# Kernel tuning notes

Hardware: AMD Instinct MI355X
Metric: run time of the kernel (lower is better)

## Reference

```python
import jax, jax.numpy as jnp
import numpy as np

NUM_HEADS = 8
DIM_IN = 512
DIM_OUT = 512


def setup_inputs() -> dict:
    key = jax.random.key(0)
    k1, k2, k3, k4, k5, k6 = jax.random.split(key, 6)
    B, T, J, C = 8, 243, 17, DIM_IN
    H = NUM_HEADS
    x = jax.random.normal(k1, (B, T, J, C), dtype=jnp.float32)
    # external attention map over temporal axis per joint: [B,H,J,T,T]
    att_map = jax.random.uniform(k2, (B, H, J, T, T), dtype=jnp.float32)
    weight = jax.random.uniform(k3, (1,), dtype=jnp.float32)
    # learned params (torch Linear stored here as [in,out] so y = x @ W)
    W_qkv = jax.random.normal(k4, (C, 3 * C), dtype=jnp.float32) * (C ** -0.5)
    W_proj = jax.random.normal(k5, (C, DIM_OUT), dtype=jnp.float32) * (C ** -0.5)
    b_proj = jax.random.normal(k6, (DIM_OUT,), dtype=jnp.float32) * 0.02
    return {"x": x, "att_map": att_map, "weight": weight,
            "W_qkv": W_qkv, "W_proj": W_proj, "b_proj": b_proj}


def reference(x, att_map, weight, W_qkv, W_proj, b_proj):
    B, T, J, C = x.shape
    H = NUM_HEADS
    hd = C // H
    scale = hd ** -0.5
    qkv = (x @ W_qkv).reshape(B, T, J, 3, H, hd)
    # permute(3,0,4,1,2,5) then transpose(2,3) -> [3,B,H,J,T,hd]
    qkv = jnp.transpose(qkv, (3, 0, 4, 2, 1, 5))
    q, k, v = qkv[0], qkv[1], qkv[2]
    attn = jax.nn.softmax(jnp.einsum('bhjtd,bhjsd->bhjts', q, k) * scale, axis=-1)
    attn = weight * attn + (1.0 - weight) * att_map  # dropout is identity (p=0 / eval)
    out = jnp.einsum('bhjts,bhjsd->bhjtd', attn, v)  # [B,H,J,T,hd]
    out = jnp.transpose(out, (0, 3, 2, 1, 4)).reshape(B, T, J, H * hd)
    return out @ W_proj + b_proj
```

## Files before the change

kernel.cpp:

```cpp
#include <hip/hip_runtime.h>
#include <hip/hip_bf16.h>
#include <cstddef>
#include <cstdint>

#define NHEADS 8
#define TT 243
#define JJ 17
#define BB 8
#define CC 512
#define HD 64
#define MROWS 33048
#define TJ 4131
#define HJ 136

typedef __attribute__((ext_vector_type(8))) short bf16x8;
typedef __attribute__((ext_vector_type(4))) float f32x4;
typedef __attribute__((ext_vector_type(4), aligned(4))) float f32x4u;

__device__ __forceinline__ unsigned short f2bf(float f) {
    return __builtin_bit_cast(unsigned short, __float2bfloat16(f));
}
__device__ __forceinline__ float b2f(unsigned short u) {
    return __uint_as_float(((unsigned)u) << 16);
}
__device__ __forceinline__ void async16(const void* g, void* l) {
    __builtin_amdgcn_global_load_lds(
        (const __attribute__((address_space(1))) void*)g,
        (__attribute__((address_space(3))) void*)l, 16, 0, 0);
}

__global__ __launch_bounds__(256) void convert_x(
    const float* __restrict__ in, unsigned short* __restrict__ out, int n4)
{
    for (int i = blockIdx.x * 256 + threadIdx.x; i < n4; i += gridDim.x * 256) {
        const float4 v = *(const float4*)(in + (size_t)i * 4);
        ushort4 o;
        o.x = f2bf(v.x); o.y = f2bf(v.y); o.z = f2bf(v.z); o.w = f2bf(v.w);
        *(ushort4*)(out + (size_t)i * 4) = o;
    }
}

__global__ __launch_bounds__(256) void transpose_w(
    const float* __restrict__ src, unsigned short* __restrict__ dst, int N)
{
    __shared__ unsigned short tile[64][65];
    const int tid = threadIdx.x;
    const int c = tid & 63, r4 = tid >> 6;
    const int n0 = blockIdx.x << 6, k0 = blockIdx.y << 6;
    #pragma unroll
    for (int p = 0; p < 16; ++p) {
        const int r = (p << 2) + r4;
        tile[r][c] = f2bf(src[(size_t)(k0 + r) * N + n0 + c]);
    }
    __syncthreads();
    #pragma unroll
    for (int p = 0; p < 16; ++p) {
        const int rr = (p << 2) + r4;
        dst[(size_t)(n0 + rr) * 512 + k0 + c] = tile[c][rr];
    }
}

__global__ __launch_bounds__(256) void gemm_qkv(
    const unsigned short* __restrict__ xb, const unsigned short* __restrict__ wt,
    unsigned short* __restrict__ qb, unsigned short* __restrict__ kb,
    unsigned short* __restrict__ vb)
{
    __shared__ __align__(16) char smem[32768];
    char* const A0 = smem;
    char* const A1 = smem + 8192;
    char* const B0 = smem + 16384;
    char* const B1 = smem + 24576;

    const int tid = threadIdx.x;
    const int wave = tid >> 6, lane = tid & 63;
    const int m0 = blockIdx.y << 7, n0 = blockIdx.x << 7;
    const int wr = wave >> 1, wc = wave & 1;

    f32x4 acc[4][4];
    #pragma unroll
    for (int i = 0; i < 4; ++i)
        #pragma unroll
        for (int j = 0; j < 4; ++j) acc[i][j] = (f32x4){0.f, 0.f, 0.f, 0.f};

    const int srow = lane >> 2;
    const int sbyte = (lane & 3) << 4;
    const int arow0 = (wave << 5) + srow;
    const int arow1 = arow0 + 16;
    const size_t am0 = (size_t)min(m0 + arow0, MROWS - 1);
    const size_t am1 = (size_t)min(m0 + arow1, MROWS - 1);
    const char* xbb = (const char*)xb;
    const char* wtb = (const char*)wt;

#define STAGEQ(Ad, Bd, k0) do { \
    async16(xbb + (am0 * 512 + (k0)) * 2 + sbyte, (Ad) + ((wave << 5) << 6)); \
    async16(xbb + (am1 * 512 + (k0)) * 2 + sbyte, (Ad) + (((wave << 5) + 16) << 6)); \
    async16(wtb + ((size_t)(n0 + arow0) * 512 + (k0)) * 2 + sbyte, (Bd) + ((wave << 5) << 6)); \
    async16(wtb + ((size_t)(n0 + arow1) * 512 + (k0)) * 2 + sbyte, (Bd) + (((wave << 5) + 16) << 6)); \
} while (0)

#define COMPUTEQ(Ap, Bp) do { \
    bf16x8 af[4], bfr[4]; \
    _Pragma("unroll") \
    for (int i = 0; i < 4; ++i) \
        af[i] = *(const bf16x8*)((const unsigned short*)(Ap) + \
            ((wr << 6) + (i << 4) + (lane & 15)) * 32 + ((lane >> 4) << 3)); \
    _Pragma("unroll") \
    for (int j = 0; j < 4; ++j) \
        bfr[j] = *(const bf16x8*)((const unsigned short*)(Bp) + \
            ((wc << 6) + (j << 4) + (lane & 15)) * 32 + ((lane >> 4) << 3)); \
    _Pragma("unroll") \
    for (int i = 0; i < 4; ++i) \
        _Pragma("unroll") \
        for (int j = 0; j < 4; ++j) \
            acc[i][j] = __builtin_amdgcn_mfma_f32_16x16x32_bf16(af[i], bfr[j], acc[i][j], 0, 0, 0); \
} while (0)

    STAGEQ(A0, B0, 0);
    __syncthreads();
    #pragma unroll
    for (int t = 0; t < 16; t += 2) {
        STAGEQ(A1, B1, (t + 1) << 5);
        COMPUTEQ(A0, B0);
        __syncthreads();
        if (t + 2 < 16) STAGEQ(A0, B0, (t + 2) << 5);
        COMPUTEQ(A1, B1);
        __syncthreads();
    }
#undef STAGEQ
#undef COMPUTEQ

    unsigned short (*Cq)[16][72] = (unsigned short (*)[16][72])smem;

    const int nw = n0 + (wc << 6);
    const int which = nw >> 9;
    const int h = (nw >> 6) & 7;
    unsigned short* const dst = which == 0 ? qb : (which == 1 ? kb : vb);
    #pragma unroll
    for (int i = 0; i < 4; ++i) {
        #pragma unroll
        for (int j = 0; j < 4; ++j)
            #pragma unroll
            for (int r = 0; r < 4; ++r)
                Cq[wave][((lane >> 4) << 2) + r][(j << 4) + (lane & 15)] = f2bf(acc[i][j][r]);
        #pragma unroll
        for (int qq = 0; qq < 4; ++qq) {
            const int rr = (qq << 2) + (lane >> 4);
            const int ch = lane & 15;
            const ushort4 val = *(const ushort4*)&Cq[wave][rr][ch << 2];
            const int m = m0 + (wr << 6) + (i << 4) + rr;
            if (m < MROWS) {
                const int b = m / TJ; const int rm = m - b * TJ;
                const int t = rm / JJ; const int jj = rm - t * JJ;
                const size_t base = (((size_t)((b * NHEADS + h) * JJ + jj) * TT + t) << 6) + (ch << 2);
                *(ushort4*)(dst + base) = val;
            }
        }
    }
}

__global__ __launch_bounds__(256) void vtrans(
    const unsigned short* __restrict__ vb, unsigned short* __restrict__ vt)
{
    __shared__ unsigned short TL[64 * 264];
    const int tid = threadIdx.x;
    const int bhj = blockIdx.x;
    const unsigned short* src = vb + (size_t)bhj * TT * HD;

    {
        const int d = tid >> 2, qq = tid & 3;
        *(ushort4*)(TL + d * 264 + 240 + (qq << 2)) = make_ushort4(0, 0, 0, 0);
    }
    __syncthreads();
    #pragma unroll
    for (int p = 0; p < 16; ++p) {
        const int idxq = tid + (p << 8);
        const int t = idxq >> 4;
        if (t < TT) {
            const int d0 = (idxq & 15) << 2;
            const ushort4 u = *(const ushort4*)(src + t * HD + d0);
            TL[(d0 + 0) * 264 + t] = u.x;
            TL[(d0 + 1) * 264 + t] = u.y;
            TL[(d0 + 2) * 264 + t] = u.z;
            TL[(d0 + 3) * 264 + t] = u.w;
        }
    }
    __syncthreads();
    unsigned short* dst = vt + ((size_t)bhj << 14);
    #pragma unroll
    for (int p = 0; p < 8; ++p) {
        const int cw = tid + (p << 8);
        const int d = cw >> 5, c = cw & 31;
        const ushort4 a = *(const ushort4*)(TL + d * 264 + (c << 3));
        const ushort4 bq = *(const ushort4*)(TL + d * 264 + (c << 3) + 4);
        *(ushort4*)(dst + (d << 8) + (c << 3)) = a;
        *(ushort4*)(dst + (d << 8) + (c << 3) + 4) = bq;
    }
}

__global__ __launch_bounds__(256, 2) void attn_mfma(
    const unsigned short* __restrict__ qb, const unsigned short* __restrict__ kb,
    const unsigned short* __restrict__ vt, const float* __restrict__ att,
    const float* __restrict__ wptr, unsigned short* __restrict__ ob)
{
    __shared__ unsigned short ST[64 * 264];

    const int tid = threadIdx.x;
    const int wave = tid >> 6, lane = tid & 63;
    const int tile = blockIdx.x & 3, bhj = blockIdx.x >> 2;
    const int row0 = tile << 6;

    const unsigned short* q = qb + (size_t)bhj * TT * HD;
    const unsigned short* k = kb + (size_t)bhj * TT * HD;
    const float* am = att + (size_t)bhj * TT * TT;
    const float w = wptr[0];

    const int lm = lane & 15, lk = lane >> 4;

    bf16x8 qf[4][2];
    #pragma unroll
    for (int mi = 0; mi < 4; ++mi) {
        const int r = min(row0 + (mi << 4) + lm, TT - 1);
        #pragma unroll
        for (int kb2 = 0; kb2 < 2; ++kb2)
            qf[mi][kb2] = *(const bf16x8*)(q + r * HD + (kb2 << 5) + (lk << 3));
    }
    bf16x8 kf[2][4];
    #pragma unroll
    for (int kb2 = 0; kb2 < 2; ++kb2)
        #pragma unroll
        for (int nj = 0; nj < 4; ++nj) {
            const int s = min((wave << 6) + (nj << 4) + lm, TT - 1);
            kf[kb2][nj] = *(const bf16x8*)(k + s * HD + (kb2 << 5) + (lk << 3));
        }

    const int row2 = tid >> 2, part = tid & 3;
    const int trow2 = row0 + row2;
    const float* amr = am + (size_t)min(trow2, TT - 1) * TT;
    float areg[15][4];
    #pragma unroll
    for (int i = 0; i < 15; ++i) {
        const f32x4u av = *(const f32x4u*)(amr + (part << 2) + (i << 4));
        areg[i][0] = av.x; areg[i][1] = av.y; areg[i][2] = av.z; areg[i][3] = av.w;
    }
    float at0 = 0.f, at1 = 0.f, at2 = 0.f;
    if (part == 0) { at0 = amr[240]; at1 = amr[241]; at2 = amr[242]; }

    f32x4 acc[4][4];
    #pragma unroll
    for (int mi = 0; mi < 4; ++mi)
        #pragma unroll
        for (int nj = 0; nj < 4; ++nj) acc[mi][nj] = (f32x4){0.f, 0.f, 0.f, 0.f};
    #pragma unroll
    for (int kb2 = 0; kb2 < 2; ++kb2)
        #pragma unroll
        for (int mi = 0; mi < 4; ++mi)
            #pragma unroll
            for (int nj = 0; nj < 4; ++nj)
                acc[mi][nj] = __builtin_amdgcn_mfma_f32_16x16x32_bf16(qf[mi][kb2], kf[kb2][nj], acc[mi][nj], 0, 0, 0);
    #pragma unroll
    for (int mi = 0; mi < 4; ++mi)
        #pragma unroll
        for (int nj = 0; nj < 4; ++nj)
            #pragma unroll
            for (int r = 0; r < 4; ++r) {
                const int m = (mi << 4) + (lk << 2) + r;
                const int s = (wave << 6) + (nj << 4) + lm;
                ST[m * 264 + s] = f2bf(acc[mi][nj][r] * 0.125f);
            }
    __syncthreads();

    {
        unsigned short* strow = ST + row2 * 264;
        if (trow2 < TT) {
            float mx = -1e30f;
            #pragma unroll
            for (int i = 0; i < 15; ++i) {
                const ushort4 u = *(const ushort4*)(strow + (part << 2) + (i << 4));
                mx = fmaxf(fmaxf(fmaxf(fmaxf(mx, b2f(u.x)), b2f(u.y)), b2f(u.z)), b2f(u.w));
            }
            if (part == 0)
                for (int s = 240; s < TT; ++s) mx = fmaxf(mx, b2f(strow[s]));
            mx = fmaxf(mx, __shfl_xor(mx, 1));
            mx = fmaxf(mx, __shfl_xor(mx, 2));

            float er[15][4];
            float l = 0.f;
            #pragma unroll
            for (int i = 0; i < 15; ++i) {
                const int s0 = (part << 2) + (i << 4);
                const ushort4 u = *(const ushort4*)(strow + s0);
                er[i][0] = __expf(b2f(u.x) - mx);
                er[i][1] = __expf(b2f(u.y) - mx);
                er[i][2] = __expf(b2f(u.z) - mx);
                er[i][3] = __expf(b2f(u.w) - mx);
                l += (er[i][0] + er[i][1]) + (er[i][2] + er[i][3]);
            }
            float et0 = 0.f, et1 = 0.f, et2 = 0.f;
            if (part == 0) {
                et0 = __expf(b2f(strow[240]) - mx);
                et1 = __expf(b2f(strow[241]) - mx);
                et2 = __expf(b2f(strow[242]) - mx);
                l += et0 + et1 + et2;
            }
            l += __shfl_xor(l, 1);
            l += __shfl_xor(l, 2);
            const float sw = w / l, aw = 1.f - w;
            #pragma unroll
            for (int i = 0; i < 15; ++i) {
                const int s0 = (part << 2) + (i << 4);
                ushort4 o;
                o.x = f2bf(er[i][0] * sw + aw * areg[i][0]);
                o.y = f2bf(er[i][1] * sw + aw * areg[i][1]);
                o.z = f2bf(er[i][2] * sw + aw * areg[i][2]);
                o.w = f2bf(er[i][3] * sw + aw * areg[i][3]);
                *(ushort4*)(strow + s0) = o;
            }
            if (part == 0) {
                strow[240] = f2bf(et0 * sw + aw * at0);
                strow[241] = f2bf(et1 * sw + aw * at1);
                strow[242] = f2bf(et2 * sw + aw * at2);
                for (int s = TT; s < 256; ++s) strow[s] = 0;
            }
        } else {
            #pragma unroll
            for (int i = 0; i < 16; ++i)
                *(ushort4*)(strow + (part << 2) + (i << 4)) = make_ushort4(0, 0, 0, 0);
        }
    }
    __syncthreads();

    f32x4 oacc[4];
    #pragma unroll
    for (int nj = 0; nj < 4; ++nj) oacc[nj] = (f32x4){0.f, 0.f, 0.f, 0.f};
    const unsigned short* strow3 = ST + ((wave << 4) + lm) * 264;
    const unsigned short* vtg = vt + ((size_t)bhj << 14);
    #pragma unroll 2
    for (int kb8 = 0; kb8 < 8; ++kb8) {
        const bf16x8 pf = *(const bf16x8*)(strow3 + (kb8 << 5) + (lk << 3));
        #pragma unroll
        for (int nj = 0; nj < 4; ++nj) {
            const int d = (nj << 4) + lm;
            const int chunk = (kb8 << 2) + lk;
            const bf16x8 vf = *(const bf16x8*)(vtg + (d << 8) + (chunk << 3));
            oacc[nj] = __builtin_amdgcn_mfma_f32_16x16x32_bf16(pf, vf, oacc[nj], 0, 0, 0);
        }
    }

    const int b = bhj / HJ;
    const int hj = bhj - b * HJ;
    const int h = hj / JJ;
    const int j = hj - h * JJ;
    #pragma unroll
    for (int r = 0; r < 4; ++r) {
        const int t = row0 + (wave << 4) + (lk << 2) + r;
        if (t < TT) {
            unsigned short* orow = ob + (((size_t)((b * TT + t) * JJ + j)) << 9) + (h << 6);
            #pragma unroll
            for (int nj = 0; nj < 4; ++nj)
                orow[(nj << 4) + lm] = f2bf(oacc[nj][r]);
        }
    }
}

__global__ __launch_bounds__(256) void gemm_proj(
    const unsigned short* __restrict__ obb, const unsigned short* __restrict__ wt,
    const float* __restrict__ bias, float* __restrict__ out)
{
    __shared__ __align__(16) char smem[32768];
    char* const A0 = smem;
    char* const A1 = smem + 8192;
    char* const B0 = smem + 16384;
    char* const B1 = smem + 24576;

    const int tid = threadIdx.x;
    const int wave = tid >> 6, lane = tid & 63;
    const int m0 = blockIdx.y << 7, n0 = blockIdx.x << 7;
    const int wr = wave >> 1, wc = wave & 1;

    f32x4 acc[4][4];
    #pragma unroll
    for (int i = 0; i < 4; ++i)
        #pragma unroll
        for (int j = 0; j < 4; ++j) acc[i][j] = (f32x4){0.f, 0.f, 0.f, 0.f};

    const int srow = lane >> 2;
    const int sbyte = (lane & 3) << 4;
    const int arow0 = (wave << 5) + srow;
    const int arow1 = arow0 + 16;
    const size_t am0 = (size_t)min(m0 + arow0, MROWS - 1);
    const size_t am1 = (size_t)min(m0 + arow1, MROWS - 1);
    const char* ab = (const char*)obb;
    const char* wtb = (const char*)wt;

#define STAGEP(Ad, Bd, k0) do { \
    async16(ab + (am0 * 512 + (k0)) * 2 + sbyte, (Ad) + ((wave << 5) << 6)); \
    async16(ab + (am1 * 512 + (k0)) * 2 + sbyte, (Ad) + (((wave << 5) + 16) << 6)); \
    async16(wtb + ((size_t)(n0 + arow0) * 512 + (k0)) * 2 + sbyte, (Bd) + ((wave << 5) << 6)); \
    async16(wtb + ((size_t)(n0 + arow1) * 512 + (k0)) * 2 + sbyte, (Bd) + (((wave << 5) + 16) << 6)); \
} while (0)

#define COMPUTEP(Ap, Bp) do { \
    bf16x8 af[4], bfr[4]; \
    _Pragma("unroll") \
    for (int i = 0; i < 4; ++i) \
        af[i] = *(const bf16x8*)((const unsigned short*)(Ap) + \
            ((wr << 6) + (i << 4) + (lane & 15)) * 32 + ((lane >> 4) << 3)); \
    _Pragma("unroll") \
    for (int j = 0; j < 4; ++j) \
        bfr[j] = *(const bf16x8*)((const unsigned short*)(Bp) + \
            ((wc << 6) + (j << 4) + (lane & 15)) * 32 + ((lane >> 4) << 3)); \
    _Pragma("unroll") \
    for (int i = 0; i < 4; ++i) \
        _Pragma("unroll") \
        for (int j = 0; j < 4; ++j) \
            acc[i][j] = __builtin_amdgcn_mfma_f32_16x16x32_bf16(af[i], bfr[j], acc[i][j], 0, 0, 0); \
} while (0)

    STAGEP(A0, B0, 0);
    __syncthreads();
    #pragma unroll
    for (int t = 0; t < 16; t += 2) {
        STAGEP(A1, B1, (t + 1) << 5);
        COMPUTEP(A0, B0);
        __syncthreads();
        if (t + 2 < 16) STAGEP(A0, B0, (t + 2) << 5);
        COMPUTEP(A1, B1);
        __syncthreads();
    }
#undef STAGEP
#undef COMPUTEP

    float (*Cp)[16][68] = (float (*)[16][68])smem;

    const int ch0 = lane & 15;
    const float4 bvec = *(const float4*)&bias[n0 + (wc << 6) + (ch0 << 2)];
    #pragma unroll
    for (int i = 0; i < 4; ++i) {
        #pragma unroll
        for (int j = 0; j < 4; ++j)
            #pragma unroll
            for (int r = 0; r < 4; ++r)
                Cp[wave][((lane >> 4) << 2) + r][(j << 4) + (lane & 15)] = acc[i][j][r];
        #pragma unroll
        for (int qq = 0; qq < 4; ++qq) {
            const int rr = (qq << 2) + (lane >> 4);
            const int ch = lane & 15;
            float4 val = *(const float4*)&Cp[wave][rr][ch << 2];
            const int m = m0 + (wr << 6) + (i << 4) + rr;
            if (m < MROWS) {
                val.x += bvec.x; val.y += bvec.y; val.z += bvec.z; val.w += bvec.w;
                *(float4*)(out + (size_t)m * 512 + n0 + (wc << 6) + (ch << 2)) = val;
            }
        }
    }
}

extern "C" void kernel_launch(void* const* d_in, const int* in_sizes, int n_in,
                              void* d_out, int out_size, void* d_ws, size_t ws_size,
                              hipStream_t stream)
{
    const float* x    = (const float*)d_in[0];
    const float* att  = (const float*)d_in[1];
    const float* wgt  = (const float*)d_in[2];
    const float* Wqkv = (const float*)d_in[3];
    const float* Wp   = (const float*)d_in[4];
    const float* bp   = (const float*)d_in[5];
    float* out = (float*)d_out;

    const size_t SZ = (size_t)MROWS * 512;
    unsigned short* xb    = (unsigned short*)d_ws;
    unsigned short* wqkvt = xb + SZ;
    unsigned short* wpt   = wqkvt + (size_t)1536 * 512;
    unsigned short* qb    = wpt + (size_t)512 * 512;
    unsigned short* kb    = qb + SZ;
    unsigned short* vb    = kb + SZ;
    unsigned short* ob    = vb + SZ;
    unsigned short* vtb   = ob + SZ;

    convert_x<<<4096, 256, 0, stream>>>(x, xb, (int)(SZ / 4));
    transpose_w<<<dim3(24, 8), 256, 0, stream>>>(Wqkv, wqkvt, 1536);
    transpose_w<<<dim3(8, 8), 256, 0, stream>>>(Wp, wpt, 512);

    gemm_qkv<<<dim3(12, 259), 256, 0, stream>>>(xb, wqkvt, qb, kb, vb);

    vtrans<<<dim3(1088), 256, 0, stream>>>(vb, vtb);

    attn_mfma<<<dim3(1088 * 4), 256, 0, stream>>>(qb, kb, vtb, att, wgt, ob);

    gemm_proj<<<dim3(4, 259), 256, 0, stream>>>(ob, wpt, bp, out);
}
```

Before: 593.8 us.

## Split attention-map blend into a second MFMA accumulation and raise occupancy

The external attention map is no longer prefetched into 60+ registers and blended into the softmax probabilities. It is now loaded per K-chunk during the PV stage, converted to bf16, and multiplied by V in a separate accumulator that is scaled by (1-w) at the end. This frees the register file so launch bounds can move from 2 to 4 blocks per SM, and the K fragments are loaded per k-block for the same reason. The trade-offs are twice the MFMA work in the PV stage, the att_map load latency now sitting inside the PV loop instead of overlapping the QK matmul, and att_map being rounded to bf16 before it is multiplied by V.

```diff
diff --git a/kernel.cpp b/kernel.cpp
--- a/kernel.cpp
+++ b/kernel.cpp
@@ -197,7 +197,7 @@
     }
 }
 
-__global__ __launch_bounds__(256, 2) void attn_mfma(
+__global__ __launch_bounds__(256, 4) void attn_mfma(
     const unsigned short* __restrict__ qb, const unsigned short* __restrict__ kb,
     const unsigned short* __restrict__ vt, const float* __restrict__ att,
     const float* __restrict__ wptr, unsigned short* __restrict__ ob)
@@ -213,6 +213,7 @@
     const unsigned short* k = kb + (size_t)bhj * TT * HD;
     const float* am = att + (size_t)bhj * TT * TT;
     const float w = wptr[0];
+    const float aw = 1.f - w;
 
     const int lm = lane & 15, lk = lane >> 4;
 
@@ -224,39 +225,25 @@
         for (int kb2 = 0; kb2 < 2; ++kb2)
             qf[mi][kb2] = *(const bf16x8*)(q + r * HD + (kb2 << 5) + (lk << 3));
     }
-    bf16x8 kf[2][4];
-    #pragma unroll
-    for (int kb2 = 0; kb2 < 2; ++kb2)
+    f32x4 acc[4][4];
+    #pragma unroll
+    for (int mi = 0; mi < 4; ++mi)
+        #pragma unroll
+        for (int nj = 0; nj < 4; ++nj) acc[mi][nj] = (f32x4){0.f, 0.f, 0.f, 0.f};
+    #pragma unroll
+    for (int kb2 = 0; kb2 < 2; ++kb2) {
+        bf16x8 kf[4];
         #pragma unroll
         for (int nj = 0; nj < 4; ++nj) {
             const int s = min((wave << 6) + (nj << 4) + lm, TT - 1);
-            kf[kb2][nj] = *(const bf16x8*)(k + s * HD + (kb2 << 5) + (lk << 3));
-        }
-
-    const int row2 = tid >> 2, part = tid & 3;
-    const int trow2 = row0 + row2;
-    const float* amr = am + (size_t)min(trow2, TT - 1) * TT;
-    float areg[15][4];
-    #pragma unroll
-    for (int i = 0; i < 15; ++i) {
-        const f32x4u av = *(const f32x4u*)(amr + (part << 2) + (i << 4));
-        areg[i][0] = av.x; areg[i][1] = av.y; areg[i][2] = av.z; areg[i][3] = av.w;
-    }
-    float at0 = 0.f, at1 = 0.f, at2 = 0.f;
-    if (part == 0) { at0 = amr[240]; at1 = amr[241]; at2 = amr[242]; }
-
-    f32x4 acc[4][4];
-    #pragma unroll
-    for (int mi = 0; mi < 4; ++mi)
-        #pragma unroll
-        for (int nj = 0; nj < 4; ++nj) acc[mi][nj] = (f32x4){0.f, 0.f, 0.f, 0.f};
-    #pragma unroll
-    for (int kb2 = 0; kb2 < 2; ++kb2)
+            kf[nj] = *(const bf16x8*)(k + s * HD + (kb2 << 5) + (lk << 3));
+        }
         #pragma unroll
         for (int mi = 0; mi < 4; ++mi)
             #pragma unroll
             for (int nj = 0; nj < 4; ++nj)
-                acc[mi][nj] = __builtin_amdgcn_mfma_f32_16x16x32_bf16(qf[mi][kb2], kf[kb2][nj], acc[mi][nj], 0, 0, 0);
+                acc[mi][nj] = __builtin_amdgcn_mfma_f32_16x16x32_bf16(qf[mi][kb2], kf[nj], acc[mi][nj], 0, 0, 0);
+    }
     #pragma unroll
     for (int mi = 0; mi < 4; ++mi)
         #pragma unroll
@@ -270,6 +257,8 @@
     __syncthreads();
 
     {
+        const int row2 = tid >> 2, part = tid & 3;
+        const int trow2 = row0 + row2;
         unsigned short* strow = ST + row2 * 264;
         if (trow2 < TT) {
             float mx = -1e30f;
@@ -304,24 +293,25 @@
             }
             l += __shfl_xor(l, 1);
             l += __shfl_xor(l, 2);
-            const float sw = w / l, aw = 1.f - w;
+            const float sw = w / l;
             #pragma unroll
             for (int i = 0; i < 15; ++i) {
                 const int s0 = (part << 2) + (i << 4);
                 ushort4 o;
-                o.x = f2bf(er[i][0] * sw + aw * areg[i][0]);
-                o.y = f2bf(er[i][1] * sw + aw * areg[i][1]);
-                o.z = f2bf(er[i][2] * sw + aw * areg[i][2]);
-                o.w = f2bf(er[i][3] * sw + aw * areg[i][3]);
+                o.x = f2bf(er[i][0] * sw);
+                o.y = f2bf(er[i][1] * sw);
+                o.z = f2bf(er[i][2] * sw);
+                o.w = f2bf(er[i][3] * sw);
                 *(ushort4*)(strow + s0) = o;
             }
             if (part == 0) {
-                strow[240] = f2bf(et0 * sw + aw * at0);
-                strow[241] = f2bf(et1 * sw + aw * at1);
-                strow[242] = f2bf(et2 * sw + aw * at2);
+                strow[240] = f2bf(et0 * sw);
+                strow[241] = f2bf(et1 * sw);
+                strow[242] = f2bf(et2 * sw);
                 for (int s = TT; s < 256; ++s) strow[s] = 0;
             }
         } else {
+            const int part = tid & 3;
             #pragma unroll
             for (int i = 0; i < 16; ++i)
                 *(ushort4*)(strow + (part << 2) + (i << 4)) = make_ushort4(0, 0, 0, 0);
@@ -329,20 +319,54 @@
     }
     __syncthreads();
 
-    f32x4 oacc[4];
-    #pragma unroll
-    for (int nj = 0; nj < 4; ++nj) oacc[nj] = (f32x4){0.f, 0.f, 0.f, 0.f};
-    const unsigned short* strow3 = ST + ((wave << 4) + lm) * 264;
+    f32x4 oacc[4], oaccA[4];
+    #pragma unroll
+    for (int nj = 0; nj < 4; ++nj) {
+        oacc[nj] = (f32x4){0.f, 0.f, 0.f, 0.f};
+        oaccA[nj] = (f32x4){0.f, 0.f, 0.f, 0.f};
+    }
+    const int prow = (wave << 4) + lm;
+    const unsigned short* strow3 = ST + prow * 264;
     const unsigned short* vtg = vt + ((size_t)bhj << 14);
+    const int arow = min(row0 + prow, TT - 1);
+    const float* arow_p = am + (size_t)arow * TT;
+
     #pragma unroll 2
-    for (int kb8 = 0; kb8 < 8; ++kb8) {
-        const bf16x8 pf = *(const bf16x8*)(strow3 + (kb8 << 5) + (lk << 3));
+    for (int kb8 = 0; kb8 < 7; ++kb8) {
+        const int s0 = (kb8 << 5) + (lk << 3);
+        const bf16x8 pf = *(const bf16x8*)(strow3 + s0);
+        const f32x4u a0 = *(const f32x4u*)(arow_p + s0);
+        const f32x4u a1 = *(const f32x4u*)(arow_p + s0 + 4);
+        bf16x8 af;
+        af[0] = (short)f2bf(a0.x); af[1] = (short)f2bf(a0.y);
+        af[2] = (short)f2bf(a0.z); af[3] = (short)f2bf(a0.w);
+        af[4] = (short)f2bf(a1.x); af[5] = (short)f2bf(a1.y);
+        af[6] = (short)f2bf(a1.z); af[7] = (short)f2bf(a1.w);
         #pragma unroll
         for (int nj = 0; nj < 4; ++nj) {
             const int d = (nj << 4) + lm;
             const int chunk = (kb8 << 2) + lk;
             const bf16x8 vf = *(const bf16x8*)(vtg + (d << 8) + (chunk << 3));
-            oacc[nj] = __builtin_amdgcn_mfma_f32_16x16x32_bf16(pf, vf, oacc[nj], 0, 0, 0);
+            oacc[nj]  = __builtin_amdgcn_mfma_f32_16x16x32_bf16(pf, vf, oacc[nj], 0, 0, 0);
+            oaccA[nj] = __builtin_amdgcn_mfma_f32_16x16x32_bf16(af, vf, oaccA[nj], 0, 0, 0);
+        }
+    }
+    {
+        const int s0 = (7 << 5) + (lk << 3);
+        const bf16x8 pf = *(const bf16x8*)(strow3 + s0);
+        bf16x8 af;
+        #pragma unroll
+        for (int e = 0; e < 8; ++e) {
+            const int s = s0 + e;
+            af[e] = (short)f2bf(s < TT ? arow_p[s] : 0.f);
+        }
+        #pragma unroll
+        for (int nj = 0; nj < 4; ++nj) {
+            const int d = (nj << 4) + lm;
+            const int chunk = (7 << 2) + lk;
+            const bf16x8 vf = *(const bf16x8*)(vtg + (d << 8) + (chunk << 3));
+            oacc[nj]  = __builtin_amdgcn_mfma_f32_16x16x32_bf16(pf, vf, oacc[nj], 0, 0, 0);
+            oaccA[nj] = __builtin_amdgcn_mfma_f32_16x16x32_bf16(af, vf, oaccA[nj], 0, 0, 0);
         }
     }
 
@@ -357,7 +381,7 @@
             unsigned short* orow = ob + (((size_t)((b * TT + t) * JJ + j)) << 9) + (h << 6);
             #pragma unroll
             for (int nj = 0; nj < 4; ++nj)
-                orow[(nj << 4) + lm] = f2bf(oacc[nj][r]);
+                orow[(nj << 4) + lm] = f2bf(oacc[nj][r] + aw * oaccA[nj][r]);
         }
     }
 }
```

After: 633.1 us. 1.07x slower.
